# Kernel optimization log

Hardware: AMD Instinct MI355X
Metric: run time of the kernel (lower is better)

The kernel has to match this reference:

```python
import jax, jax.numpy as jnp
import numpy as np
from jax.scipy.linalg import expm

S = 2048  # state size = 2**max_num_qubits
B = 4096  # batch


def setup_inputs() -> dict:
    key = jax.random.key(0)
    k1, k2, k3 = jax.random.split(key, 3)
    inputs = jax.random.normal(k1, (B, S), dtype=jnp.float32)
    M_real = 0.1 * jax.random.normal(k2, (S, S), dtype=jnp.float32)
    M_imag = 0.1 * jax.random.normal(k3, (S, S), dtype=jnp.float32)
    bias = jnp.zeros((S,), dtype=jnp.float32)
    qubit_gate = jnp.ones((S,), dtype=jnp.float32)
    return {"inputs": inputs, "M_real": M_real, "M_imag": M_imag,
            "bias": bias, "qubit_gate": qubit_gate}


def reference(inputs, M_real, M_imag, bias, qubit_gate):
    # l2-normalize along last axis (matches tf.linalg.l2_normalize)
    norm = jnp.sqrt(jnp.maximum(jnp.sum(inputs * inputs, axis=-1, keepdims=True), 1e-12))
    norm_inputs = inputs / norm
    # skew-symmetric generators -> orthogonal-like transforms via expm
    A = M_real - M_real.T
    Bm = M_imag - M_imag.T
    U = expm(A) @ expm(Bm)
    transformed = norm_inputs @ U + bias  # [B, S]
    measured = jnp.square(transformed)
    gate_probs = jax.nn.softmax(qubit_gate)  # [S]
    gated_output = measured * gate_probs
    return gated_output, gate_probs
```

## Files before the change

### kernel.cpp

```cpp
#include <hip/hip_runtime.h>
#include <math.h>

#define SD 2048
#define BDIM 4096

typedef _Float16 f16;
using f16x8 = __attribute__((ext_vector_type(8))) f16;
using f32x4 = __attribute__((ext_vector_type(4))) float;

#define EPS_CROSS 4.8828125e-4f
#define LSCALE    2048.0f

__device__ __forceinline__ void fsplit(float x, f16& h, f16& l) {
    h = (f16)x;
    l = (f16)((x - (float)h) * LSCALE);
}
__device__ __forceinline__ float fcomb(f16 h, f16 l) {
    return (float)h + (float)l * EPS_CROSS;
}
__device__ __forceinline__ void glds16(const void* g, void* l) {
    __builtin_amdgcn_global_load_lds(
        (const __attribute__((address_space(1))) unsigned int*)g,
        (__attribute__((address_space(3))) unsigned int*)l, 16, 0, 0);
}

struct GArgs {
    const f16 *Ah, *Al, *Bh, *Bl;
    f16 *CAh, *CAl; float sA, dA;
    f16 *C2h, *C2l; float s2, d2;
    f16 *CBh, *CBl; float sB, dB;
    float *C32; const float *bias, *gate;
};

template<int OUT>
__global__ __launch_bounds__(256, 2)
void gsplit_k(GArgs gz0, GArgs gz1)
{
    const GArgs g = blockIdx.z ? gz1 : gz0;
    __shared__ char smem[65536];
    const int tid  = threadIdx.x;
    const int lane = tid & 63, wid = tid >> 6;
    const int row0 = blockIdx.y * 128, col0 = blockIdx.x * 128;

    const int lrow = lane >> 2;
    const int gsl  = (lane & 3) ^ ((lrow >> 1) & 3);
    const f16* splane = (wid == 0) ? g.Ah : (wid == 1) ? g.Al
                      : (wid == 2) ? g.Bh : g.Bl;
    const int  sbase  = (wid < 2) ? row0 : col0;
    const size_t sgoff = (size_t)(sbase + lrow) * SD + gsl * 8;

    auto stage = [&](int buf, int k0) {
        char* lb = smem + buf * 32768 + wid * 8192;
        const f16* gp = splane + sgoff + k0;
        #pragma unroll
        for (int s = 0; s < 8; ++s)
            glds16(gp + (size_t)s * 16 * SD, lb + s * 1024);
    };

    const int lr = lane & 15, lg = lane >> 4;
    const int wm = wid >> 1, wn = wid & 1;
    const int afo = (wm*64 + lr)*64 + ((lg ^ ((lr >> 1) & 3)) << 4);
    const int bfo = (wn*64 + lr)*64 + ((lg ^ ((lr >> 1) & 3)) << 4);

    f32x4 ch[4][4], cx[4][4];
    #pragma unroll
    for (int m = 0; m < 4; ++m)
    #pragma unroll
    for (int n = 0; n < 4; ++n) { ch[m][n] = (f32x4)0.f; cx[m][n] = (f32x4)0.f; }

    stage(0, 0);
    stage(1, 32);
    for (int kt = 0; kt < 64; ++kt) {
        const int cur = kt & 1;
        if (kt < 63) asm volatile("s_waitcnt vmcnt(8)" ::: "memory");
        else         asm volatile("s_waitcnt vmcnt(0)" ::: "memory");
        __builtin_amdgcn_s_barrier();

        const char* base = smem + cur * 32768;
        f16x8 ah[4], al[4], bh[4], bl[4];
        #pragma unroll
        for (int m = 0; m < 4; ++m) {
            ah[m] = *(const f16x8*)(base +     0 + afo + m*1024);
            al[m] = *(const f16x8*)(base +  8192 + afo + m*1024);
        }
        #pragma unroll
        for (int n = 0; n < 4; ++n) {
            bh[n] = *(const f16x8*)(base + 16384 + bfo + n*1024);
            bl[n] = *(const f16x8*)(base + 24576 + bfo + n*1024);
        }
        #pragma unroll
        for (int m = 0; m < 4; ++m)
        #pragma unroll
        for (int n = 0; n < 4; ++n) {
            ch[m][n] = __builtin_amdgcn_mfma_f32_16x16x32_f16(ah[m], bh[n], ch[m][n], 0, 0, 0);
            cx[m][n] = __builtin_amdgcn_mfma_f32_16x16x32_f16(ah[m], bl[n], cx[m][n], 0, 0, 0);
            cx[m][n] = __builtin_amdgcn_mfma_f32_16x16x32_f16(al[m], bh[n], cx[m][n], 0, 0, 0);
        }

        __builtin_amdgcn_s_barrier();
        if (kt + 2 < 64) stage(cur, (kt + 2) * 32);
    }

    const int erow = wm*64 + lg*4;
    const int ecol = wn*64 + lr;

    if (OUT == 0) {
        f16* lds16 = (f16*)smem;
        auto dumpPlane = [&](f16* dst, bool transp) {
            #pragma unroll
            for (int i = 0; i < 8; ++i) {
                int chunk = i * 256 + tid;
                int r = chunk >> 4, cs = chunk & 15;
                f16x8 v = *(const f16x8*)(lds16 + r * 136 + cs * 8);
                size_t go = transp ? ((size_t)(col0 + r) * SD + row0 + cs * 8)
                                   : ((size_t)(row0 + r) * SD + col0 + cs * 8);
                *(f16x8*)(dst + go) = v;
            }
        };
        auto writePair = [&](f16* dh, f16* dl, float s, float d, bool transp) {
            #pragma unroll
            for (int pl = 0; pl < 2; ++pl) {
                __syncthreads();
                #pragma unroll
                for (int m = 0; m < 4; ++m)
                #pragma unroll
                for (int n = 0; n < 4; ++n)
                #pragma unroll
                for (int q = 0; q < 4; ++q) {
                    int rl = erow + m*16 + q, cl = ecol + n*16;
                    float v  = ch[m][n][q] + EPS_CROSS * cx[m][n][q];
                    float vv = s * v + (((row0 + rl) == (col0 + cl)) ? d : 0.f);
                    f16 h, l; fsplit(vv, h, l);
                    int idx = transp ? (cl * 136 + rl) : (rl * 136 + cl);
                    lds16[idx] = pl ? l : h;
                }
                __syncthreads();
                dumpPlane(pl ? dl : dh, transp);
            }
        };
        if (g.CAh) writePair(g.CAh, g.CAl, g.sA, g.dA, false);
        if (g.C2h) writePair(g.C2h, g.C2l, g.s2, g.d2, false);
        if (g.CBh) writePair(g.CBh, g.CBl, g.sB, g.dB, true);
    } else {
        float* lds32 = (float*)smem;
        #pragma unroll
        for (int h = 0; h < 2; ++h) {
            __syncthreads();
            if (wn == h) {
                #pragma unroll
                for (int m = 0; m < 4; ++m)
                #pragma unroll
                for (int n = 0; n < 4; ++n) {
                    int cl = ecol + n*16;
                    float b  = g.bias[col0 + cl];
                    float ga = g.gate[col0 + cl];
                    #pragma unroll
                    for (int q = 0; q < 4; ++q) {
                        int rl = erow + m*16 + q;
                        float v = ch[m][n][q] + EPS_CROSS * cx[m][n][q];
                        float t = v + b;
                        lds32[rl*68 + (cl - h*64)] = t * t * ga;
                    }
                }
            }
            __syncthreads();
            #pragma unroll
            for (int i = 0; i < 8; ++i) {
                int chunk = i * 256 + tid;
                int r = chunk >> 4, cs = chunk & 15;
                float4 v = *(const float4*)(lds32 + r*68 + cs*4);
                *(float4*)(g.C32 + (size_t)(row0 + r) * SD + col0 + h*64 + cs*4) = v;
            }
        }
    }
}

struct SArgs { const float* M; f16 *XAh, *XAl, *XBh, *XBl; };

__global__ __launch_bounds__(256)
void skew_split_k(SArgs sz0, SArgs sz1, float scale)
{
    const SArgs s = blockIdx.z ? sz1 : sz0;
    __shared__ float t1[32][33], t2[32][33];
    const int bx = blockIdx.x*32, by = blockIdx.y*32;
    const int tx = threadIdx.x, ty = threadIdx.y;
    #pragma unroll
    for (int r = 0; r < 32; r += 8) {
        t1[ty+r][tx] = s.M[(size_t)(by+ty+r)*SD + bx+tx];
        t2[ty+r][tx] = s.M[(size_t)(bx+ty+r)*SD + by+tx];
    }
    __syncthreads();
    #pragma unroll
    for (int r = 0; r < 32; r += 8) {
        float xs = (t1[ty+r][tx] - t2[tx][ty+r]) * scale;
        size_t idx = (size_t)(by+ty+r)*SD + bx+tx;
        f16 h, l;
        fsplit(xs, h, l);  s.XAh[idx] = h; s.XAl[idx] = l;
        fsplit(-xs, h, l); s.XBh[idx] = h; s.XBl[idx] = l;
    }
}

struct EArgs { const float* M; float cA; f16 *Ahp, *Alp; float cB; f16 *Bhp, *Blp; };

__global__ __launch_bounds__(256)
void eadd_k(EArgs ez0, EArgs ez1, float scale)
{
    const EArgs e = blockIdx.z ? ez1 : ez0;
    __shared__ float t1[32][33], t2[32][33];
    const int bx = blockIdx.x*32, by = blockIdx.y*32;
    const int tx = threadIdx.x, ty = threadIdx.y;
    #pragma unroll
    for (int r = 0; r < 32; r += 8) {
        t1[ty+r][tx] = e.M[(size_t)(by+ty+r)*SD + bx+tx];
        t2[ty+r][tx] = e.M[(size_t)(bx+ty+r)*SD + by+tx];
    }
    __syncthreads();
    #pragma unroll
    for (int r = 0; r < 32; r += 8) {
        float xs = (t1[ty+r][tx] - t2[tx][ty+r]) * scale;
        size_t idx = (size_t)(by+ty+r)*SD + bx+tx;
        f16 h, l;
        float va = fcomb(e.Ahp[idx], e.Alp[idx]) + e.cA * xs;
        fsplit(va, h, l); e.Ahp[idx] = h; e.Alp[idx] = l;
        if (e.Bhp) {
            float vb = fcomb(e.Bhp[idx], e.Blp[idx]) + e.cB * xs;
            fsplit(vb, h, l); e.Bhp[idx] = h; e.Blp[idx] = l;
        }
    }
}

__global__ __launch_bounds__(256)
void rownorm_k(const float* __restrict__ in, float* __restrict__ rn)
{
    const int row = blockIdx.x;
    const float4* p = (const float4*)(in + (size_t)row * SD);
    float ss = 0.f;
    for (int i = threadIdx.x; i < SD / 4; i += 256) {
        float4 v = p[i];
        ss += v.x*v.x + v.y*v.y + v.z*v.z + v.w*v.w;
    }
#pragma unroll
    for (int o = 32; o; o >>= 1) ss += __shfl_down(ss, o);
    __shared__ float part[4];
    if ((threadIdx.x & 63) == 0) part[threadIdx.x >> 6] = ss;
    __syncthreads();
    if (threadIdx.x == 0) {
        const float t = part[0] + part[1] + part[2] + part[3];
        rn[row] = 1.0f / sqrtf(fmaxf(t, 1e-12f));
    }
}

__global__ __launch_bounds__(256)
void nsplit_k(const float* __restrict__ in, const float* __restrict__ rn,
              f16* __restrict__ ph, f16* __restrict__ pl)
{
    const size_t gid  = (size_t)blockIdx.x * 256 + threadIdx.x;
    const size_t base = gid * 8;
    const float r = rn[(int)(base >> 11)];
    float4 a = *(const float4*)(in + base);
    float4 b = *(const float4*)(in + base + 4);
    float v[8] = {a.x, a.y, a.z, a.w, b.x, b.y, b.z, b.w};
    f16x8 h, l;
    #pragma unroll
    for (int j = 0; j < 8; ++j) {
        f16 hh, ll; fsplit(v[j] * r, hh, ll);
        h[j] = hh; l[j] = ll;
    }
    *(f16x8*)(ph + base) = h;
    *(f16x8*)(pl + base) = l;
}

__global__ __launch_bounds__(256)
void softmax_k(const float* __restrict__ q, float* __restrict__ pws,
               float* __restrict__ pout)
{
    __shared__ float red[4];
    const int tid = threadIdx.x;
    float m = -INFINITY;
    for (int i = tid; i < SD; i += 256) m = fmaxf(m, q[i]);
#pragma unroll
    for (int o = 32; o; o >>= 1) m = fmaxf(m, __shfl_down(m, o));
    if ((tid & 63) == 0) red[tid >> 6] = m;
    __syncthreads();
    const float gm = fmaxf(fmaxf(red[0], red[1]), fmaxf(red[2], red[3]));
    float s = 0.f;
    for (int i = tid; i < SD; i += 256) s += expf(q[i] - gm);
#pragma unroll
    for (int o = 32; o; o >>= 1) s += __shfl_down(s, o);
    __syncthreads();
    if ((tid & 63) == 0) red[tid >> 6] = s;
    __syncthreads();
    const float inv = 1.0f / (red[0] + red[1] + red[2] + red[3]);
    for (int i = tid; i < SD; i += 256) {
        const float val = expf(q[i] - gm) * inv;
        pws[i] = val;
        pout[i] = val;
    }
}

struct Pair { f16* h; f16* l; };

static GArgs mkG(Pair A, Pair B, Pair CA, float sA, float dA,
                 Pair C2, float s2, float d2, Pair CB, float sB, float dB)
{
    GArgs g{};
    g.Ah = A.h; g.Al = A.l; g.Bh = B.h; g.Bl = B.l;
    g.CAh = CA.h; g.CAl = CA.l; g.sA = sA; g.dA = dA;
    g.C2h = C2.h; g.C2l = C2.l; g.s2 = s2; g.d2 = d2;
    g.CBh = CB.h; g.CBl = CB.l; g.sB = sB; g.dB = dB;
    g.C32 = nullptr; g.bias = nullptr; g.gate = nullptr;
    return g;
}

struct ChainBuf { Pair p[4]; const float* Msrc; bool finalB; };

#define SC (1.0f / 16.0f)

static void expm_sched(hipStream_t st, int nz, const ChainBuf& c0, const ChainBuf& c1)
{
    const float k2 = 0.5f, k3 = 1.f/6.f, k4 = 1.f/24.f, k5 = 1.f/120.f, k6 = 1.f/720.f;
    const Pair NP{nullptr, nullptr};
    const dim3 tb(256);
    const dim3 gsq(SD/128, SD/128, nz);
    const dim3 gtr(SD/32, SD/32, nz), ttr(32, 8);

    auto G = [&](GArgs a, GArgs b) { gsplit_k<0><<<gsq, tb, 0, st>>>(a, b); };
    auto E = [&](EArgs a, EArgs b) { eadd_k<<<gtr, ttr, 0, st>>>(a, b, SC); };

    SArgs s0{c0.Msrc, c0.p[0].h, c0.p[0].l, c0.p[1].h, c0.p[1].l};
    SArgs s1{c1.Msrc, c1.p[0].h, c1.p[0].l, c1.p[1].h, c1.p[1].l};
    skew_split_k<<<gtr, ttr, 0, st>>>(s0, s1, SC);

    auto g1 = [&](const ChainBuf& c) {
        return mkG(c.p[0], c.p[1], c.p[2], k6, k4, c.p[3], 1.f, 0.f, NP, 0.f, 0.f); };
    G(g1(c0), g1(c1));
    auto e1 = [&](const ChainBuf& c) {
        return EArgs{c.Msrc, k5, c.p[2].h, c.p[2].l, 0.f, nullptr, nullptr}; };
    E(e1(c0), e1(c1));
    auto g2 = [&](const ChainBuf& c) {
        return mkG(c.p[2], c.p[3], c.p[0], 1.f, k2, NP, 0.f, 0.f, NP, 0.f, 0.f); };
    G(g2(c0), g2(c1));
    auto e2 = [&](const ChainBuf& c) {
        return EArgs{c.Msrc, k3, c.p[0].h, c.p[0].l, 0.f, nullptr, nullptr}; };
    E(e2(c0), e2(c1));
    auto g3 = [&](const ChainBuf& c) {
        return mkG(c.p[0], c.p[3], c.p[1], 1.f, 1.f, NP, 0.f, 0.f, c.p[2], 1.f, 1.f); };
    G(g3(c0), g3(c1));
    auto e3 = [&](const ChainBuf& c) {
        return EArgs{c.Msrc, 1.f, c.p[1].h, c.p[1].l, -1.f, c.p[2].h, c.p[2].l}; };
    E(e3(c0), e3(c1));

    auto sqF = [&](const ChainBuf& c, int ia, int ib, int oa, int ob) {
        return mkG(c.p[ia], c.p[ib], c.p[oa], 1.f, 0.f, NP, 0.f, 0.f, c.p[ob], 1.f, 0.f); };
    G(sqF(c0, 1, 2, 0, 3), sqF(c1, 1, 2, 0, 3));
    G(sqF(c0, 0, 3, 1, 2), sqF(c1, 0, 3, 1, 2));
    G(sqF(c0, 1, 2, 0, 3), sqF(c1, 1, 2, 0, 3));
    auto sqL = [&](const ChainBuf& c) {
        Pair ca = c.finalB ? NP : c.p[1];
        Pair cb = c.finalB ? c.p[1] : NP;
        return mkG(c.p[0], c.p[3], ca, 1.f, 0.f, NP, 0.f, 0.f, cb, 1.f, 0.f); };
    G(sqL(c0), sqL(c1));
}

extern "C" void kernel_launch(void* const* d_in, const int* in_sizes, int n_in,
                              void* d_out, int out_size, void* d_ws, size_t ws_size,
                              hipStream_t stream)
{
    const float* inputs = (const float*)d_in[0];
    const float* Mr     = (const float*)d_in[1];
    const float* Mi     = (const float*)d_in[2];
    const float* bias   = (const float*)d_in[3];
    const float* qg     = (const float*)d_in[4];
    float* out = (float*)d_out;

    const size_t PLANE = (size_t)SD * SD * sizeof(f16);
    const size_t PAIRB = 2 * PLANE;
    char* wsb = (char*)d_ws;
    char* ob  = (char*)d_out;

    auto WP = [&](int i) { char* b = wsb + (size_t)i * PAIRB;
                           return Pair{(f16*)b, (f16*)(b + PLANE)}; };
    auto DP = [&](int i) { char* b = ob + (size_t)i * PAIRB;
                           return Pair{(f16*)b, (f16*)(b + PLANE)}; };

    const bool fused = ws_size >= 6 * PAIRB + 64 * 1024;
    const size_t smallOff = (fused ? 6 : 3) * PAIRB;
    float* rnorm = (float*)(wsb + smallOff);
    float* gatew = rnorm + 4096;
    float* gout  = out + (size_t)BDIM * SD;

    const dim3 tb256(256);
    const dim3 gsq1(SD/128, SD/128, 1);
    const dim3 gbt(SD/128, BDIM/128, 1);

    rownorm_k<<<BDIM, tb256, 0, stream>>>(inputs, rnorm);
    softmax_k<<<1, tb256, 0, stream>>>(qg, gatew, gout);

    Pair EA, EB, UF;
    int ninSlotA, ninSlotB;
    if (fused) {
        ChainBuf c0{{WP(0), WP(1), WP(2), WP(3)}, Mr, false};
        ChainBuf c1{{WP(4), WP(5), DP(0), DP(1)}, Mi, true};
        expm_sched(stream, 2, c0, c1);
        EA = WP(1); EB = WP(5); UF = WP(0);
        ninSlotA = 2; ninSlotB = 3;
    } else {
        ChainBuf c0{{WP(0), WP(1), DP(0), DP(1)}, Mr, false};
        expm_sched(stream, 1, c0, c0);
        ChainBuf c1{{WP(0), WP(2), DP(0), DP(1)}, Mi, true};
        expm_sched(stream, 1, c1, c1);
        EA = WP(1); EB = WP(2); UF = WP(0);
        ninSlotA = 1; ninSlotB = 2;
    }

    {
        GArgs u = mkG(EA, EB, Pair{nullptr,nullptr}, 0.f, 0.f,
                      Pair{nullptr,nullptr}, 0.f, 0.f, UF, 1.f, 0.f);
        gsplit_k<0><<<gsq1, tb256, 0, stream>>>(u, u);
    }
    f16* ninh = (f16*)(wsb + (size_t)ninSlotA * PAIRB);
    f16* ninl = (f16*)(wsb + (size_t)ninSlotB * PAIRB);
    nsplit_k<<<(BDIM * SD / 8) / 256, tb256, 0, stream>>>(inputs, rnorm, ninh, ninl);
    {
        GArgs b{};
        b.Ah = ninh; b.Al = ninl;
        b.Bh = UF.h; b.Bl = UF.l;
        b.C32 = out; b.bias = bias; b.gate = gatew;
        gsplit_k<2><<<gbt, tb256, 0, stream>>>(b, b);
    }

    (void)in_sizes; (void)n_in; (void)out_size;
}
```

Measured before the change: 1.165 ms.

## Load B low plane directly to registers and remap workgroups across XCDs

The B low-order plane is now loaded straight from global memory into registers and double-buffered across iterations, instead of being staged through LDS. This cuts LDS use per block from 64KB to 48KB, which may allow more resident blocks, and removes LDS reads for that plane. A workgroup-id swizzle also interleaves tiles across the 8 XCDs to improve L2 locality. The trade-offs are extra register pressure and direct global loads whose latency the MFMA work has to hide, with vmcnt waits retuned to match.

```diff
diff --git a/kernel.cpp b/kernel.cpp
--- a/kernel.cpp
+++ b/kernel.cpp
@@ -37,30 +37,43 @@
 void gsplit_k(GArgs gz0, GArgs gz1)
 {
     const GArgs g = blockIdx.z ? gz1 : gz0;
-    __shared__ char smem[65536];
+    __shared__ char smem[49152];
     const int tid  = threadIdx.x;
     const int lane = tid & 63, wid = tid >> 6;
-    const int row0 = blockIdx.y * 128, col0 = blockIdx.x * 128;
+
+    const int gx = gridDim.x, nwg = gx * gridDim.y;
+    int id = blockIdx.x + gx * blockIdx.y;
+    id = (id & 7) * (nwg >> 3) + (id >> 3);
+    const int bx = id % gx, by = id / gx;
+    const int row0 = by * 128, col0 = bx * 128;
 
     const int lrow = lane >> 2;
     const int gsl  = (lane & 3) ^ ((lrow >> 1) & 3);
-    const f16* splane = (wid == 0) ? g.Ah : (wid == 1) ? g.Al
-                      : (wid == 2) ? g.Bh : g.Bl;
-    const int  sbase  = (wid < 2) ? row0 : col0;
-    const size_t sgoff = (size_t)(sbase + lrow) * SD + gsl * 8;
 
     auto stage = [&](int buf, int k0) {
-        char* lb = smem + buf * 32768 + wid * 8192;
-        const f16* gp = splane + sgoff + k0;
-        #pragma unroll
-        for (int s = 0; s < 8; ++s)
-            glds16(gp + (size_t)s * 16 * SD, lb + s * 1024);
+        #pragma unroll
+        for (int j = 0; j < 6; ++j) {
+            const int c = wid * 6 + j;
+            const int p = c >> 3, s = c & 7;
+            const f16* pb = (p == 0) ? g.Ah : (p == 1) ? g.Al : g.Bh;
+            const int  rb = (p < 2) ? row0 : col0;
+            const f16* gp = pb + (size_t)(rb + s * 16 + lrow) * SD + gsl * 8 + k0;
+            glds16(gp, smem + buf * 24576 + p * 8192 + s * 1024);
+        }
     };
 
     const int lr = lane & 15, lg = lane >> 4;
     const int wm = wid >> 1, wn = wid & 1;
-    const int afo = (wm*64 + lr)*64 + ((lg ^ ((lr >> 1) & 3)) << 4);
-    const int bfo = (wn*64 + lr)*64 + ((lg ^ ((lr >> 1) & 3)) << 4);
+    const int sxo = (lg ^ ((lr >> 1) & 3)) << 4;
+    const int afo = (wm * 64 + lr) * 64 + sxo;
+    const int bfo = (wn * 64 + lr) * 64 + sxo;
+
+    auto loadBL = [&](int k0, f16x8* d) {
+        #pragma unroll
+        for (int n = 0; n < 4; ++n)
+            d[n] = *(const f16x8*)(g.Bl +
+                (size_t)(col0 + wn * 64 + n * 16 + lr) * SD + k0 + lg * 8);
+    };
 
     f32x4 ch[4][4], cx[4][4];
     #pragma unroll
@@ -68,41 +81,49 @@
     #pragma unroll
     for (int n = 0; n < 4; ++n) { ch[m][n] = (f32x4)0.f; cx[m][n] = (f32x4)0.f; }
 
+    f16x8 blA[4], blB[4];
     stage(0, 0);
+    loadBL(0, blA);
     stage(1, 32);
-    for (int kt = 0; kt < 64; ++kt) {
+
+    auto body = [&](int kt, f16x8* use, f16x8* pre) {
         const int cur = kt & 1;
-        if (kt < 63) asm volatile("s_waitcnt vmcnt(8)" ::: "memory");
-        else         asm volatile("s_waitcnt vmcnt(0)" ::: "memory");
+        if (kt < 63) asm volatile("s_waitcnt vmcnt(10)" ::: "memory");
+        else         asm volatile("s_waitcnt vmcnt(4)"  ::: "memory");
         __builtin_amdgcn_s_barrier();
 
-        const char* base = smem + cur * 32768;
-        f16x8 ah[4], al[4], bh[4], bl[4];
+        const char* base = smem + cur * 24576;
+        f16x8 ah[4], al[4], bh[4];
         #pragma unroll
         for (int m = 0; m < 4; ++m) {
-            ah[m] = *(const f16x8*)(base +     0 + afo + m*1024);
-            al[m] = *(const f16x8*)(base +  8192 + afo + m*1024);
+            ah[m] = *(const f16x8*)(base +    0 + afo + m * 1024);
+            al[m] = *(const f16x8*)(base + 8192 + afo + m * 1024);
         }
         #pragma unroll
+        for (int n = 0; n < 4; ++n)
+            bh[n] = *(const f16x8*)(base + 16384 + bfo + n * 1024);
+
+        #pragma unroll
+        for (int m = 0; m < 4; ++m)
+        #pragma unroll
         for (int n = 0; n < 4; ++n) {
-            bh[n] = *(const f16x8*)(base + 16384 + bfo + n*1024);
-            bl[n] = *(const f16x8*)(base + 24576 + bfo + n*1024);
+            ch[m][n] = __builtin_amdgcn_mfma_f32_16x16x32_f16(ah[m], bh[n],  ch[m][n], 0, 0, 0);
+            cx[m][n] = __builtin_amdgcn_mfma_f32_16x16x32_f16(ah[m], use[n], cx[m][n], 0, 0, 0);
+            cx[m][n] = __builtin_amdgcn_mfma_f32_16x16x32_f16(al[m], bh[n],  cx[m][n], 0, 0, 0);
         }
-        #pragma unroll
-        for (int m = 0; m < 4; ++m)
-        #pragma unroll
-        for (int n = 0; n < 4; ++n) {
-            ch[m][n] = __builtin_amdgcn_mfma_f32_16x16x32_f16(ah[m], bh[n], ch[m][n], 0, 0, 0);
-            cx[m][n] = __builtin_amdgcn_mfma_f32_16x16x32_f16(ah[m], bl[n], cx[m][n], 0, 0, 0);
-            cx[m][n] = __builtin_amdgcn_mfma_f32_16x16x32_f16(al[m], bh[n], cx[m][n], 0, 0, 0);
-        }
 
         __builtin_amdgcn_s_barrier();
+        if (kt + 1 < 64) loadBL((kt + 1) * 32, pre);
         if (kt + 2 < 64) stage(cur, (kt + 2) * 32);
-    }
-
-    const int erow = wm*64 + lg*4;
-    const int ecol = wn*64 + lr;
+    };
+
+    for (int k2 = 0; k2 < 64; k2 += 2) {
+        body(k2,     blA, blB);
+        body(k2 + 1, blB, blA);
+    }
+
+    const int erow = wm * 64 + lg * 4;
+    const int ecol = wn * 64 + lr;
 
     if (OUT == 0) {
         f16* lds16 = (f16*)smem;
@@ -127,7 +148,7 @@
                 for (int n = 0; n < 4; ++n)
                 #pragma unroll
                 for (int q = 0; q < 4; ++q) {
-                    int rl = erow + m*16 + q, cl = ecol + n*16;
+                    int rl = erow + m * 16 + q, cl = ecol + n * 16;
                     float v  = ch[m][n][q] + EPS_CROSS * cx[m][n][q];
                     float vv = s * v + (((row0 + rl) == (col0 + cl)) ? d : 0.f);
                     f16 h, l; fsplit(vv, h, l);
@@ -151,15 +172,15 @@
                 for (int m = 0; m < 4; ++m)
                 #pragma unroll
                 for (int n = 0; n < 4; ++n) {
-                    int cl = ecol + n*16;
+                    int cl = ecol + n * 16;
                     float b  = g.bias[col0 + cl];
                     float ga = g.gate[col0 + cl];
                     #pragma unroll
                     for (int q = 0; q < 4; ++q) {
-                        int rl = erow + m*16 + q;
+                        int rl = erow + m * 16 + q;
                         float v = ch[m][n][q] + EPS_CROSS * cx[m][n][q];
                         float t = v + b;
-                        lds32[rl*68 + (cl - h*64)] = t * t * ga;
+                        lds32[rl * 68 + (cl - h * 64)] = t * t * ga;
                     }
                 }
             }
@@ -168,8 +189,8 @@
             for (int i = 0; i < 8; ++i) {
                 int chunk = i * 256 + tid;
                 int r = chunk >> 4, cs = chunk & 15;
-                float4 v = *(const float4*)(lds32 + r*68 + cs*4);
-                *(float4*)(g.C32 + (size_t)(row0 + r) * SD + col0 + h*64 + cs*4) = v;
+                float4 v = *(const float4*)(lds32 + r * 68 + cs * 4);
+                *(float4*)(g.C32 + (size_t)(row0 + r) * SD + col0 + h * 64 + cs * 4) = v;
             }
         }
     }
```

Result: slower. 1.315 ms (+12.9%).
